# Optimization experiments

Hardware: AMD Instinct MI355X
Metric: run time of the kernel (lower is better)

Reference implementation:

```python
import jax, jax.numpy as jnp
import numpy as np

D_MODEL = 1024
NHEAD = 16
HEAD_DIM = D_MODEL // NHEAD
D_FF = 4096
EPS = 1e-5


def _layer_norm(x, g, b):
    mu = jnp.mean(x, axis=-1, keepdims=True)
    var = jnp.mean((x - mu) ** 2, axis=-1, keepdims=True)
    return (x - mu) * jax.lax.rsqrt(var + EPS) * g + b


def _rotate_every_two(x):
    x1 = x[..., ::2]
    x2 = x[..., 1::2]
    return jnp.stack([-x2, x1], axis=-1).reshape(x.shape)


def _rope_cos_sin(pos_start, length, head_dim, dtype):
    inv_freq = 1.0 / (10000.0 ** (jnp.arange(0, head_dim, 2, dtype=jnp.float32) / head_dim))
    pos = jnp.arange(pos_start, pos_start + length, dtype=jnp.float32)
    ang = jnp.einsum('i,j->ij', pos, inv_freq)  # (len, head_dim/2)
    cos = jnp.repeat(jnp.cos(ang), 2, axis=-1).astype(dtype)
    sin = jnp.repeat(jnp.sin(ang), 2, axis=-1).astype(dtype)
    return cos, sin


def setup_inputs() -> dict:
    key = jax.random.key(0)
    ks = jax.random.split(key, 16)
    s = 1.0 / np.sqrt(D_MODEL)
    sf = 1.0 / np.sqrt(D_FF)
    inp = {
        'src': jax.random.normal(ks[0], (2048, 2, D_MODEL), jnp.float32),
        'src_mask': jnp.ones((2048, 2048), jnp.float32),
        'Wq': jax.random.normal(ks[1], (D_MODEL, D_MODEL), jnp.float32) * s,
        'bq': jnp.zeros((D_MODEL,), jnp.float32),
        'Wk': jax.random.normal(ks[2], (D_MODEL, D_MODEL), jnp.float32) * s,
        'bk': jnp.zeros((D_MODEL,), jnp.float32),
        'Wv': jax.random.normal(ks[3], (D_MODEL, D_MODEL), jnp.float32) * s,
        'bv': jnp.zeros((D_MODEL,), jnp.float32),
        'Wo': jax.random.normal(ks[4], (D_MODEL, D_MODEL), jnp.float32) * s,
        'bo': jnp.zeros((D_MODEL,), jnp.float32),
        'W1': jax.random.normal(ks[5], (D_MODEL, D_FF), jnp.float32) * s,
        'b1': jnp.zeros((D_FF,), jnp.float32),
        'W2': jax.random.normal(ks[6], (D_FF, D_MODEL), jnp.float32) * sf,
        'b2': jnp.zeros((D_MODEL,), jnp.float32),
        'g1': jnp.ones((D_MODEL,), jnp.float32),
        'be1': jnp.zeros((D_MODEL,), jnp.float32),
        'g2': jnp.ones((D_MODEL,), jnp.float32),
        'be2': jnp.zeros((D_MODEL,), jnp.float32),
    }
    return inp


def _attention(q, k, v, attn_mask):
    # q, k, v: (S, B, D) already projected
    s, b, _ = q.shape
    kl = k.shape[0]

    def heads(x):
        # (L, B, D) -> (B, H, L, dh)
        return x.reshape(x.shape[0], b, NHEAD, HEAD_DIM).transpose(1, 2, 0, 3)

    qh, kh, vh = heads(q), heads(k), heads(v)
    q_cos, q_sin = _rope_cos_sin(0, s, HEAD_DIM, qh.dtype)
    k_cos, k_sin = _rope_cos_sin(0, kl, HEAD_DIM, kh.dtype)
    qh = qh * q_cos + _rotate_every_two(qh) * q_sin
    kh = kh * k_cos + _rotate_every_two(kh) * k_sin

    scores = jnp.einsum('bhqd,bhkd->bhqk', qh, kh) / np.sqrt(HEAD_DIM)
    if attn_mask is not None:
        scores = jnp.where(attn_mask[None, None, :, :] < 0.1, -jnp.inf, scores)
    w = jax.nn.softmax(scores, axis=-1)
    out = jnp.einsum('bhqk,bhkd->bhqd', w, vh)  # (B, H, S, dh)
    out = out.transpose(2, 0, 1, 3).reshape(s, b, D_MODEL)
    return out


def reference(src, src_mask, Wq, bq, Wk, bk, Wv, bv, Wo, bo, W1, b1, W2, b2, g1, be1, g2, be2):
    q = src @ Wq + bq
    k = src @ Wk + bk
    v = src @ Wv + bv
    attn = _attention(q, k, v, src_mask) @ Wo + bo
    src2 = _layer_norm(src + attn, g1, be1)
    ff = jax.nn.relu(src2 @ W1 + b1) @ W2 + b2
    out = _layer_norm(src2 + ff, g2, be2)
    return out
```

## Files before the change

kernel.cpp:

```cpp
#include <hip/hip_runtime.h>
#include <math.h>

#define S_LEN 2048
#define DM 1024
#define NH 16
#define HD 64
#define DFF 4096
#define MROWS 4096

typedef unsigned short u16;
typedef __attribute__((ext_vector_type(8))) __bf16 bf16x8;
typedef __attribute__((ext_vector_type(4))) float f32x4;
typedef __attribute__((ext_vector_type(16))) float f32x16;
typedef __attribute__((ext_vector_type(4))) int int32x4;

__device__ __forceinline__ u16 f2bf(float f) {
  unsigned u = __float_as_uint(f);
  unsigned r = (u + 0x7fffu + ((u >> 16) & 1u)) >> 16;
  return (u16)r;
}

__device__ __forceinline__ float bf2f(u16 u) {
  return __uint_as_float((unsigned)u << 16);
}

__device__ __forceinline__ unsigned cvtpk_bf16(float lo, float hi) {
  unsigned r;
  asm("v_cvt_pk_bf16_f32 %0, %1, %2" : "=v"(r) : "v"(lo), "v"(hi));
  return r;
}

__device__ __forceinline__ void gload_lds16(const void* g, void* l) {
  __builtin_amdgcn_global_load_lds((__attribute__((address_space(1))) void*)g,
                                   (__attribute__((address_space(3))) void*)l, 16, 0, 0);
}

__global__ __launch_bounds__(256) void k_prep(const float* __restrict__ Wq, const float* __restrict__ Wk,
                                              const float* __restrict__ Wv, const float* __restrict__ Wo,
                                              const float* __restrict__ W1, const float* __restrict__ W2,
                                              u16* __restrict__ Wq_t, u16* __restrict__ Wk_t,
                                              u16* __restrict__ Wv_t, u16* __restrict__ Wo_t,
                                              u16* __restrict__ W1_t, u16* __restrict__ W2_t,
                                              const float4* __restrict__ src4, ushort4* __restrict__ Xbf4) {
  int flat = blockIdx.x;
  if (flat >= 12288) {
    int i = (flat - 12288) * 256 + threadIdx.x;
    float4 v = src4[i];
    ushort4 o;
    o.x = f2bf(v.x); o.y = f2bf(v.y); o.z = f2bf(v.z); o.w = f2bf(v.w);
    Xbf4[i] = o;
    return;
  }
  __shared__ float tile[32][33];
  const float* W;
  u16* Wt;
  int local, nx, K, N;
  if (flat < 4096) {
    int z = flat >> 10;
    W = z == 0 ? Wq : z == 1 ? Wk : z == 2 ? Wv : Wo;
    Wt = z == 0 ? Wq_t : z == 1 ? Wk_t : z == 2 ? Wv_t : Wo_t;
    local = flat & 1023; nx = 32; K = 1024; N = 1024;
  } else if (flat < 8192) {
    W = W1; Wt = W1_t; local = flat - 4096; nx = 128; K = 1024; N = 4096;
  } else {
    W = W2; Wt = W2_t; local = flat - 8192; nx = 32; K = 4096; N = 1024;
  }
  int n0 = (local % nx) * 32, k0 = (local / nx) * 32;
  int tx = threadIdx.x & 31, ty = threadIdx.x >> 5;
  #pragma unroll
  for (int r = ty; r < 32; r += 8) tile[r][tx] = W[(size_t)(k0 + r) * N + n0 + tx];
  __syncthreads();
  #pragma unroll
  for (int r = ty; r < 32; r += 8) Wt[(size_t)(n0 + r) * K + k0 + tx] = f2bf(tile[tx][r]);
}

__global__ __launch_bounds__(256) void k_misc(float* __restrict__ cosT, float* __restrict__ sinT,
                                              const float* __restrict__ bq, const float* __restrict__ bk,
                                              const float* __restrict__ bv, float* __restrict__ bqkv,
                                              const float* __restrict__ mask,
                                              unsigned char* __restrict__ flags) {
  int flat = blockIdx.x;
  if (flat < 256) {
    int idx = flat * 256 + threadIdx.x;
    int s = idx >> 5, i = idx & 31;
    float inv = powf(10000.f, -(float)(2 * i) / 64.f);
    float ang = (float)s * inv;
    cosT[idx] = cosf(ang);
    sinT[idx] = sinf(ang);
    return;
  }
  if (flat < 268) {
    int i = (flat - 256) * 256 + threadIdx.x;
    if (i < 3072) bqkv[i] = i < 1024 ? bq[i] : (i < 2048 ? bk[i - 1024] : bv[i - 2048]);
    return;
  }
  int local = flat - 268;
  int kt = local & 31, qt = local >> 5;
  const float* mp = mask + (size_t)(qt * 64) * S_LEN + kt * 64;
  int tr = threadIdx.x >> 2;
  int tc = (threadIdx.x & 3) * 16;
  int ok = 1;
  #pragma unroll
  for (int c = 0; c < 16; c += 4) {
    float4 v = *(const float4*)(mp + (size_t)tr * S_LEN + tc + c);
    ok &= (v.x >= 0.1f) & (v.y >= 0.1f) & (v.z >= 0.1f) & (v.w >= 0.1f);
  }
  ok = __all(ok) ? 1 : 0;
  __shared__ int sh[4];
  if ((threadIdx.x & 63) == 0) sh[threadIdx.x >> 6] = ok;
  __syncthreads();
  if (threadIdx.x == 0) flags[qt * 32 + kt] = (sh[0] & sh[1] & sh[2] & sh[3]) ? 0 : 1;
}

enum { EPI_F32 = 0, EPI_RELU_BF16 = 2, EPI_PARTB = 4, EPI_BF16 = 5 };

template <int EPI>
__global__ __launch_bounds__(512, 2) void k_gemm256(const u16* __restrict__ A,
                                                    const u16* __restrict__ Bt,
                                                    const float* __restrict__ bias,
                                                    float* __restrict__ Cf, u16* __restrict__ Cb,
                                                    int M, int N, int K, int ldc, int Kc) {
  __shared__ __attribute__((aligned(16))) u16 As[4][256 * 32];
  __shared__ __attribute__((aligned(16))) u16 Bs[4][256 * 32];

  int nx = gridDim.x;
  int nwg = nx * gridDim.y;
  int flat = blockIdx.y * nx + blockIdx.x;
  int id = (flat & 7) * (nwg >> 3) + (flat >> 3);
  int n0 = (id % nx) * 256;
  int m0 = (id / nx) * 256;
  int kz = blockIdx.z * Kc;

  int tid = threadIdx.x;
  int lane = tid & 63, w = tid >> 6;
  int wm = (w >> 2) * 128, wn = (w & 3) * 64;
  int l15 = lane & 15, l4 = lane >> 4;
  int NT = Kc >> 5;

  const u16* aS[2];
  const u16* bS[2];
  int dslot[2];
  #pragma unroll
  for (int j = 0; j < 2; ++j) {
    int P = j * 512 + tid;
    int r = P >> 2;
    int sl = (P & 3) ^ (r & 3);
    aS[j] = A + (size_t)(m0 + r) * K + kz + sl * 8;
    bS[j] = Bt + (size_t)(n0 + r) * K + kz + sl * 8;
    dslot[j] = j * 512 + w * 64;
  }

  f32x4 acc[8][4] = {};

  #pragma unroll
  for (int t = 0; t < 3; ++t) {
    #pragma unroll
    for (int j = 0; j < 2; ++j) {
      gload_lds16(aS[j] + t * 32, &As[t][dslot[j] * 8]);
      gload_lds16(bS[j] + t * 32, &Bs[t][dslot[j] * 8]);
    }
  }

  for (int t = 0; t < NT; ++t) {
    int buf = t & 3;
    if (t < NT - 2) asm volatile("s_waitcnt vmcnt(8)" ::: "memory");
    else if (t == NT - 2) asm volatile("s_waitcnt vmcnt(4)" ::: "memory");
    else asm volatile("s_waitcnt vmcnt(0)" ::: "memory");
    __builtin_amdgcn_s_barrier();

    if (t + 3 < NT) {
      int tn = t + 3;
      int bn = tn & 3;
      #pragma unroll
      for (int j = 0; j < 2; ++j) {
        gload_lds16(aS[j] + tn * 32, &As[bn][dslot[j] * 8]);
        gload_lds16(bS[j] + tn * 32, &Bs[bn][dslot[j] * 8]);
      }
    }

    bf16x8 af[8], bq[4];
    #pragma unroll
    for (int m = 0; m < 8; ++m) {
      int r = wm + m * 16 + l15;
      af[m] = *(const bf16x8*)&As[buf][r * 32 + (l4 ^ (r & 3)) * 8];
    }
    #pragma unroll
    for (int n = 0; n < 4; ++n) {
      int r = wn + n * 16 + l15;
      bq[n] = *(const bf16x8*)&Bs[buf][r * 32 + (l4 ^ (r & 3)) * 8];
    }
    __builtin_amdgcn_s_setprio(1);
    #pragma unroll
    for (int m = 0; m < 8; ++m)
      #pragma unroll
      for (int n = 0; n < 4; ++n)
        acc[m][n] = __builtin_amdgcn_mfma_f32_16x16x32_bf16(af[m], bq[n], acc[m][n], 0, 0, 0);
    __builtin_amdgcn_s_setprio(0);
  }

  size_t zoff = (size_t)blockIdx.z * M * ldc;
  #pragma unroll
  for (int m = 0; m < 8; ++m) {
    #pragma unroll
    for (int n = 0; n < 4; ++n) {
      int col = n0 + wn + n * 16 + l15;
      float bv = (EPI == EPI_PARTB) ? 0.f : bias[col];
      #pragma unroll
      for (int r = 0; r < 4; ++r) {
        int row = m0 + wm + m * 16 + l4 * 4 + r;
        float v = acc[m][n][r] + bv;
        size_t o = (size_t)row * ldc + col;
        if (EPI == EPI_F32) Cf[o] = v;
        else if (EPI == EPI_RELU_BF16) Cb[o] = f2bf(fmaxf(v, 0.f));
        else if (EPI == EPI_BF16) Cb[o] = f2bf(v);
        else Cb[zoff + o] = f2bf(v);
      }
    }
  }
}

#define QSCALE 0.180336881f
__global__ __launch_bounds__(256) void k_rope_heads(const u16* __restrict__ QKVb,
                                                    const float* __restrict__ cosT,
                                                    const float* __restrict__ sinT,
                                                    u16* __restrict__ Qh, u16* __restrict__ Kh,
                                                    u16* __restrict__ Vt) {
  __shared__ u16 Vlds[64 * 80];
  int bh = blockIdx.y;
  int s0 = blockIdx.x * 64;
  int b = bh >> 4, h = bh & 15;
  int tid = threadIdx.x;
  int sr = tid >> 2, dg = (tid & 3) * 16;
  int s = s0 + sr;
  size_t rowbase = (size_t)(s * 2 + b) * 3072 + h * 64 + dg;

  float4 c0 = *(const float4*)&cosT[s * 32 + (dg >> 1)];
  float4 c1 = *(const float4*)&cosT[s * 32 + (dg >> 1) + 4];
  float4 sn0 = *(const float4*)&sinT[s * 32 + (dg >> 1)];
  float4 sn1 = *(const float4*)&sinT[s * 32 + (dg >> 1) + 4];
  float cs[8] = {c0.x, c0.y, c0.z, c0.w, c1.x, c1.y, c1.z, c1.w};
  float sn[8] = {sn0.x, sn0.y, sn0.z, sn0.w, sn1.x, sn1.y, sn1.z, sn1.w};

  {
    uint4 a = *(const uint4*)&QKVb[rowbase];
    uint4 bbu = *(const uint4*)&QKVb[rowbase + 8];
    unsigned ws[8] = {a.x, a.y, a.z, a.w, bbu.x, bbu.y, bbu.z, bbu.w};
    unsigned o[8];
    #pragma unroll
    for (int j = 0; j < 8; ++j) {
      float lo = bf2f((u16)(ws[j] & 0xffff)), hi = bf2f((u16)(ws[j] >> 16));
      o[j] = cvtpk_bf16((lo * cs[j] - hi * sn[j]) * QSCALE, (hi * cs[j] + lo * sn[j]) * QSCALE);
    }
    u16* qp = &Qh[((size_t)bh * S_LEN + s) * 64 + dg];
    *(uint4*)qp = (uint4){o[0], o[1], o[2], o[3]};
    *(uint4*)(qp + 8) = (uint4){o[4], o[5], o[6], o[7]};
  }
  {
    uint4 a = *(const uint4*)&QKVb[rowbase + 1024];
    uint4 bbu = *(const uint4*)&QKVb[rowbase + 1032];
    unsigned ws[8] = {a.x, a.y, a.z, a.w, bbu.x, bbu.y, bbu.z, bbu.w};
    unsigned o[8];
    #pragma unroll
    for (int j = 0; j < 8; ++j) {
      float lo = bf2f((u16)(ws[j] & 0xffff)), hi = bf2f((u16)(ws[j] >> 16));
      o[j] = cvtpk_bf16(lo * cs[j] - hi * sn[j], hi * cs[j] + lo * sn[j]);
    }
    u16* kp = &Kh[((size_t)bh * S_LEN + s) * 64 + dg];
    *(uint4*)kp = (uint4){o[0], o[1], o[2], o[3]};
    *(uint4*)(kp + 8) = (uint4){o[4], o[5], o[6], o[7]};
  }
  {
    uint4 a = *(const uint4*)&QKVb[rowbase + 2048];
    uint4 bbu = *(const uint4*)&QKVb[rowbase + 2056];
    unsigned ws[8] = {a.x, a.y, a.z, a.w, bbu.x, bbu.y, bbu.z, bbu.w};
    #pragma unroll
    for (int j = 0; j < 8; ++j) {
      Vlds[(dg + 2 * j) * 80 + sr] = (u16)(ws[j] & 0xffff);
      Vlds[(dg + 2 * j + 1) * 80 + sr] = (u16)(ws[j] >> 16);
    }
  }
  __syncthreads();
  {
    int d = tid >> 2, sg = (tid & 3) * 16;
    uint4 v0 = *(const uint4*)&Vlds[d * 80 + sg];
    uint4 v1 = *(const uint4*)&Vlds[d * 80 + sg + 8];
    u16* vp = &Vt[((size_t)bh * 64 + d) * S_LEN + s0 + sg];
    *(uint4*)vp = v0;
    *(uint4*)(vp + 8) = v1;
  }
}

__global__ __launch_bounds__(256) void k_attn(const u16* __restrict__ Qh, const u16* __restrict__ Kh,
                                              const u16* __restrict__ Vt,
                                              const float* __restrict__ mask,
                                              const unsigned char* __restrict__ flags,
                                              u16* __restrict__ Out) {
  __shared__ __attribute__((aligned(16))) u16 Ks[2][128 * 64];
  __shared__ __attribute__((aligned(16))) u16 Vs[2][64 * 128];
  int f = blockIdx.y * gridDim.x + blockIdx.x;
  int xcd = f & 7, ii = f >> 3;
  int bh = xcd * 4 + (ii >> 4);
  int q0 = (ii & 15) * 128;
  int b = bh >> 4, h = bh & 15;
  int tid = threadIdx.x, lane = tid & 63, w = tid >> 6;
  int l31 = lane & 31, l5 = lane >> 5;

  int qrow = q0 + w * 32 + l31;
  int qt = qrow >> 6;

  bf16x8 qf[4];
  {
    const u16* qp = Qh + ((size_t)bh * S_LEN + qrow) * 64 + l5 * 8;
    #pragma unroll
    for (int dc = 0; dc < 4; ++dc) qf[dc] = *(const bf16x8*)(qp + dc * 16);
  }

  const u16* Kbase = Kh + (size_t)bh * S_LEN * 64;
  const u16* Vbase = Vt + (size_t)bh * 64 * S_LEN;

  int ksid[4], vsid[4];
  const u16* kg[4];
  const u16* vg[4];
  #pragma unroll
  for (int i = 0; i < 4; ++i) {
    int sid = i * 256 + tid;
    ksid[i] = sid;
    int kr = sid >> 3, kslot = sid & 7;
    kg[i] = Kbase + (size_t)kr * 64 + (kslot ^ (kr & 7)) * 8;
    vsid[i] = sid;
    int vr = sid >> 4, vslot = sid & 15;
    vg[i] = Vbase + (size_t)vr * S_LEN + ((vslot ^ (vr & 15))) * 8;
  }

  float m_run = -1e30f, l_run = 0.f;
  f32x16 oA = {}, oB = {};

  const int NTILE = S_LEN / 128;
  #pragma unroll
  for (int i = 0; i < 4; ++i) {
    gload_lds16(kg[i], &Ks[0][ksid[i] * 8]);
    gload_lds16(vg[i], &Vs[0][vsid[i] * 8]);
  }

  for (int t = 0; t < NTILE; ++t) {
    int cur = t & 1;
    int kv0 = t * 128;
    asm volatile("s_waitcnt vmcnt(0)" ::: "memory");
    __builtin_amdgcn_s_barrier();
    if (t + 1 < NTILE) {
      int kvn = (t + 1) * 128;
      #pragma unroll
      for (int i = 0; i < 4; ++i) {
        gload_lds16(kg[i] + (size_t)kvn * 64, &Ks[cur ^ 1][ksid[i] * 8]);
        gload_lds16(vg[i] + kvn, &Vs[cur ^ 1][vsid[i] * 8]);
      }
    }

    #pragma unroll
    for (int ksub = 0; ksub < 2; ++ksub) {
      int koff = ksub * 64;
      f32x16 sA = {}, sB = {};
      __builtin_amdgcn_s_setprio(1);
      #pragma unroll
      for (int dc = 0; dc < 4; ++dc) {
        int r0 = koff + l31;
        int r1 = koff + 32 + l31;
        int slot = (dc * 2 + l5) ^ (l31 & 7);
        bf16x8 ka0 = *(const bf16x8*)&Ks[cur][r0 * 64 + slot * 8];
        bf16x8 ka1 = *(const bf16x8*)&Ks[cur][r1 * 64 + slot * 8];
        sA = __builtin_amdgcn_mfma_f32_32x32x16_bf16(ka0, qf[dc], sA, 0, 0, 0);
        sB = __builtin_amdgcn_mfma_f32_32x32x16_bf16(ka1, qf[dc], sB, 0, 0, 0);
      }
      __builtin_amdgcn_s_setprio(0);

      int fl = flags[qt * 32 + ((kv0 + koff) >> 6)];
      if (fl) {
        const float* mrow = mask + (size_t)qrow * S_LEN + kv0 + koff;
        #pragma unroll
        for (int r = 0; r < 16; ++r) {
          int key = (r & 3) + 8 * (r >> 2) + 4 * l5;
          if (mrow[key] < 0.1f) sA[r] = -1e30f;
          if (mrow[key + 32] < 0.1f) sB[r] = -1e30f;
        }
      }

      float pm = m_run;
      #pragma unroll
      for (int r = 0; r < 16; ++r) pm = fmaxf(pm, fmaxf(sA[r], sB[r]));
      pm = fmaxf(pm, __shfl_xor(pm, 32, 64));
      if (!__all(pm <= m_run + 8.f)) {
        float corr = __builtin_amdgcn_exp2f(m_run - pm);
        m_run = pm;
        l_run *= corr;
        #pragma unroll
        for (int r = 0; r < 16; ++r) { oA[r] *= corr; oB[r] *= corr; }
      }
      float ps = 0.f;
      #pragma unroll
      for (int r = 0; r < 16; ++r) {
        sA[r] = __builtin_amdgcn_exp2f(sA[r] - m_run);
        sB[r] = __builtin_amdgcn_exp2f(sB[r] - m_run);
        ps += sA[r] + sB[r];
      }
      l_run += ps;

      __builtin_amdgcn_s_setprio(1);
      #pragma unroll
      for (int kh = 0; kh < 2; ++kh) {
        f32x16 s = kh ? sB : sA;
        #pragma unroll
        for (int c = 0; c < 2; ++c) {
          int base = c * 8;
          unsigned u0 = cvtpk_bf16(s[base + 0], s[base + 1]);
          unsigned u1 = cvtpk_bf16(s[base + 2], s[base + 3]);
          unsigned u2 = cvtpk_bf16(s[base + 4], s[base + 5]);
          unsigned u3 = cvtpk_bf16(s[base + 6], s[base + 7]);
          asm volatile("v_permlane32_swap_b32 %0, %1" : "+v"(u0), "+v"(u2));
          asm volatile("v_permlane32_swap_b32 %0, %1" : "+v"(u1), "+v"(u3));
          int32x4 wds = {(int)u0, (int)u1, (int)u2, (int)u3};
          bf16x8 pb = *(bf16x8*)&wds;
          int kslot = ksub * 8 + (kh * 2 + c) * 2 + l5;
          int vr0 = l31, vr1 = 32 + l31;
          bf16x8 va0 = *(const bf16x8*)&Vs[cur][vr0 * 128 + (kslot ^ (vr0 & 15)) * 8];
          bf16x8 va1 = *(const bf16x8*)&Vs[cur][vr1 * 128 + (kslot ^ (vr1 & 15)) * 8];
          oA = __builtin_amdgcn_mfma_f32_32x32x16_bf16(va0, pb, oA, 0, 0, 0);
          oB = __builtin_amdgcn_mfma_f32_32x32x16_bf16(va1, pb, oB, 0, 0, 0);
        }
      }
      __builtin_amdgcn_s_setprio(0);
    }
  }

  float l_tot = l_run + __shfl_xor(l_run, 32, 64);
  float inv = 1.f / l_tot;
  int mrow = qrow * 2 + b;
  u16* op = Out + (size_t)mrow * DM + h * 64;
  #pragma unroll
  for (int db = 0; db < 2; ++db) {
    f32x16 o = db ? oB : oA;
    #pragma unroll
    for (int g = 0; g < 4; ++g) {
      int d0 = db * 32 + 8 * g + 4 * l5;
      ushort4 st;
      st.x = f2bf(o[4 * g + 0] * inv);
      st.y = f2bf(o[4 * g + 1] * inv);
      st.z = f2bf(o[4 * g + 2] * inv);
      st.w = f2bf(o[4 * g + 3] * inv);
      *(ushort4*)(op + d0) = st;
    }
  }
}

__device__ __forceinline__ float wave_sum(float v) {
  #pragma unroll
  for (int off = 32; off >= 1; off >>= 1) v += __shfl_xor(v, off, 64);
  return v;
}

template <int WB>
__global__ __launch_bounds__(256) void k_lnp(const u16* __restrict__ pb, const float* __restrict__ addf,
                                             const float* __restrict__ bvec,
                                             const float* __restrict__ gw, const float* __restrict__ bw,
                                             float* __restrict__ Yf, u16* __restrict__ Yb) {
  int m = blockIdx.x;
  int tid = threadIdx.x, lane = tid & 63, w = tid >> 6;
  __shared__ float part[4];
  __shared__ float shv[2];
  float4 sc = ((const float4*)(addf + (size_t)m * DM))[tid];
  float4 bv = ((const float4*)bvec)[tid];
  float vx = sc.x + bv.x, vy = sc.y + bv.y, vz = sc.z + bv.z, vw = sc.w + bv.w;
  #pragma unroll
  for (int z = 0; z < 4; ++z) {
    ushort4 qv = ((const ushort4*)(pb + (size_t)z * MROWS * DM + (size_t)m * DM))[tid];
    vx += bf2f(qv.x); vy += bf2f(qv.y); vz += bf2f(qv.z); vw += bf2f(qv.w);
  }
  float s = wave_sum(vx + vy + vz + vw);
  if (lane == 0) part[w] = s;
  __syncthreads();
  if (tid == 0) shv[0] = (part[0] + part[1] + part[2] + part[3]) * (1.f / DM);
  __syncthreads();
  float mu = shv[0];
  float d0 = vx - mu, d1 = vy - mu, d2 = vz - mu, d3 = vw - mu;
  float q = wave_sum(d0 * d0 + d1 * d1 + d2 * d2 + d3 * d3);
  if (lane == 0) part[w] = q;
  __syncthreads();
  if (tid == 0) shv[1] = rsqrtf((part[0] + part[1] + part[2] + part[3]) * (1.f / DM) + 1e-5f);
  __syncthreads();
  float rstd = shv[1];
  float4 g4 = ((const float4*)gw)[tid];
  float4 b4 = ((const float4*)bw)[tid];
  float y0 = d0 * rstd * g4.x + b4.x;
  float y1 = d1 * rstd * g4.y + b4.y;
  float y2 = d2 * rstd * g4.z + b4.z;
  float y3 = d3 * rstd * g4.w + b4.w;
  ((float4*)(Yf + (size_t)m * DM))[tid] = make_float4(y0, y1, y2, y3);
  if (WB) {
    ushort4 o;
    o.x = f2bf(y0); o.y = f2bf(y1); o.z = f2bf(y2); o.w = f2bf(y3);
    ((ushort4*)(Yb + (size_t)m * DM))[tid] = o;
  }
}

extern "C" void kernel_launch(void* const* d_in, const int* in_sizes, int n_in,
                              void* d_out, int out_size, void* d_ws, size_t ws_size,
                              hipStream_t stream) {
  (void)in_sizes; (void)n_in; (void)out_size; (void)ws_size;
  const float* src  = (const float*)d_in[0];
  const float* mask = (const float*)d_in[1];
  const float* Wq = (const float*)d_in[2];  const float* bq  = (const float*)d_in[3];
  const float* Wk = (const float*)d_in[4];  const float* bk  = (const float*)d_in[5];
  const float* Wv = (const float*)d_in[6];  const float* bv  = (const float*)d_in[7];
  const float* Wo = (const float*)d_in[8];  const float* bo  = (const float*)d_in[9];
  const float* W1 = (const float*)d_in[10]; const float* b1  = (const float*)d_in[11];
  const float* W2 = (const float*)d_in[12]; const float* b2  = (const float*)d_in[13];
  const float* g1 = (const float*)d_in[14]; const float* be1 = (const float*)d_in[15];
  const float* g2 = (const float*)d_in[16]; const float* be2 = (const float*)d_in[17];
  float* out = (float*)d_out;

  char* base = (char*)d_ws;
  size_t off = 0;
  auto carve = [&](size_t bytes) -> void* {
    void* r = base + off;
    off += (bytes + 255) & ~(size_t)255;
    return r;
  };
  u16* Wq_t = (u16*)carve(2ull * 1024 * 1024);
  u16* Wk_t = (u16*)carve(2ull * 1024 * 1024);
  u16* Wv_t = (u16*)carve(2ull * 1024 * 1024);
  u16* Wo_t = (u16*)carve(2ull * 1024 * 1024);
  u16* W1_t = (u16*)carve(2ull * 4096 * 1024);
  u16* W2_t = (u16*)carve(2ull * 1024 * 4096);
  u16* Xbf  = (u16*)carve(2ull * 4096 * 1024);
  float* cosT = (float*)carve(4ull * 2048 * 32);
  float* sinT = (float*)carve(4ull * 2048 * 32);
  float* bqkv = (float*)carve(4ull * 3072);
  unsigned char* mflags = (unsigned char*)carve(1024);
  u16* attn_out = (u16*)carve(2ull * 4096 * 1024);
  float* src2f = (float*)carve(4ull * 4096 * 1024);
  float* QKV = (float*)carve(4ull * 4096 * 3072);
  u16* Qh = (u16*)carve(2ull * 32 * 2048 * 64);
  u16* Kh = (u16*)carve(2ull * 32 * 2048 * 64);
  u16* Vt = (u16*)carve(2ull * 32 * 2048 * 64);
  u16* QKVb = (u16*)QKV;
  u16* woPb = (u16*)QKV;
  u16* ff1 = (u16*)QKV;
  u16* ffPb = (u16*)((char*)QKV + 32ull * 1024 * 1024);
  u16* src2b = (u16*)Vt;

  dim3 blk(256);
  dim3 blk5(512);
  k_prep<<<dim3(16384), blk, 0, stream>>>(Wq, Wk, Wv, Wo, W1, W2, Wq_t, Wk_t, Wv_t, Wo_t,
                                          W1_t, W2_t, (const float4*)src, (ushort4*)Xbf);
  k_misc<<<dim3(1292), blk, 0, stream>>>(cosT, sinT, bq, bk, bv, bqkv, mask, mflags);
  k_gemm256<EPI_BF16><<<dim3(12, 16, 1), blk5, 0, stream>>>(Xbf, Wq_t, bqkv, nullptr, QKVb, 4096, 3072, 1024, 3072, 1024);
  k_rope_heads<<<dim3(32, 32), blk, 0, stream>>>(QKVb, cosT, sinT, Qh, Kh, Vt);
  k_attn<<<dim3(16, 32), blk, 0, stream>>>(Qh, Kh, Vt, mask, mflags, attn_out);
  k_gemm256<EPI_PARTB><<<dim3(4, 16, 4), blk5, 0, stream>>>(attn_out, Wo_t, nullptr, nullptr, woPb, 4096, 1024, 1024, 1024, 256);
  k_lnp<1><<<dim3(4096), blk, 0, stream>>>(woPb, src, bo, g1, be1, src2f, src2b);
  k_gemm256<EPI_RELU_BF16><<<dim3(16, 16, 1), blk5, 0, stream>>>(src2b, W1_t, b1, nullptr, ff1, 4096, 4096, 1024, 4096, 1024);
  k_gemm256<EPI_PARTB><<<dim3(4, 16, 4), blk5, 0, stream>>>(ff1, W2_t, nullptr, nullptr, ffPb, 4096, 1024, 4096, 1024, 1024);
  k_lnp<0><<<dim3(4096), blk, 0, stream>>>(ffPb, src2f, b2, g2, be2, out, nullptr);
}
```

Before: 278.1 us.

## Split attention KV tile across two wave groups with LDS merge of partial softmax

The attention kernel now runs 512 threads per block. Two groups of four waves each process one 64-key half of every 128-key tile for the same 128 query rows. The groups keep separate online-softmax state and merge their max, sum and output accumulators through LDS at the end. The global-to-LDS loads are split across the larger block, and the max and sum reductions are tree-shaped. The aim is more waves in flight and shorter dependent chains per tile, at the cost of a final cross-group merge, extra barriers and register pressure under launch_bounds(512,2).

```diff
diff --git a/kernel.cpp b/kernel.cpp
--- a/kernel.cpp
+++ b/kernel.cpp
@@ -290,11 +290,11 @@
   }
 }
 
-__global__ __launch_bounds__(256) void k_attn(const u16* __restrict__ Qh, const u16* __restrict__ Kh,
-                                              const u16* __restrict__ Vt,
-                                              const float* __restrict__ mask,
-                                              const unsigned char* __restrict__ flags,
-                                              u16* __restrict__ Out) {
+__global__ __launch_bounds__(512, 2) void k_attn(const u16* __restrict__ Qh, const u16* __restrict__ Kh,
+                                                 const u16* __restrict__ Vt,
+                                                 const float* __restrict__ mask,
+                                                 const unsigned char* __restrict__ flags,
+                                                 u16* __restrict__ Out) {
   __shared__ __attribute__((aligned(16))) u16 Ks[2][128 * 64];
   __shared__ __attribute__((aligned(16))) u16 Vs[2][64 * 128];
   int f = blockIdx.y * gridDim.x + blockIdx.x;
@@ -303,9 +303,10 @@
   int q0 = (ii & 15) * 128;
   int b = bh >> 4, h = bh & 15;
   int tid = threadIdx.x, lane = tid & 63, w = tid >> 6;
+  int wq = w & 3, wh = w >> 2;
   int l31 = lane & 31, l5 = lane >> 5;
 
-  int qrow = q0 + w * 32 + l31;
+  int qrow = q0 + wq * 32 + l31;
   int qt = qrow >> 6;
 
   bf16x8 qf[4];
@@ -318,18 +319,14 @@
   const u16* Kbase = Kh + (size_t)bh * S_LEN * 64;
   const u16* Vbase = Vt + (size_t)bh * 64 * S_LEN;
 
-  int ksid[4], vsid[4];
-  const u16* kg[4];
-  const u16* vg[4];
-  #pragma unroll
-  for (int i = 0; i < 4; ++i) {
-    int sid = i * 256 + tid;
-    ksid[i] = sid;
-    int kr = sid >> 3, kslot = sid & 7;
-    kg[i] = Kbase + (size_t)kr * 64 + (kslot ^ (kr & 7)) * 8;
-    vsid[i] = sid;
-    int vr = sid >> 4, vslot = sid & 15;
-    vg[i] = Vbase + (size_t)vr * S_LEN + ((vslot ^ (vr & 15))) * 8;
+  int koff_[2], voff_[2];
+  #pragma unroll
+  for (int i = 0; i < 2; ++i) {
+    int s = i * 512 + tid;
+    int kr = s >> 3, kslot = s & 7;
+    koff_[i] = kr * 64 + (kslot ^ (kr & 7)) * 8;
+    int vr = s >> 4, vslot = s & 15;
+    voff_[i] = vr * S_LEN + (vslot ^ (vr & 15)) * 8;
   }
 
   float m_run = -1e30f, l_run = 0.f;
@@ -337,116 +334,144 @@
 
   const int NTILE = S_LEN / 128;
   #pragma unroll
-  for (int i = 0; i < 4; ++i) {
-    gload_lds16(kg[i], &Ks[0][ksid[i] * 8]);
-    gload_lds16(vg[i], &Vs[0][vsid[i] * 8]);
-  }
+  for (int i = 0; i < 2; ++i) {
+    gload_lds16(Kbase + koff_[i], &Ks[0][(i * 512 + tid) * 8]);
+    gload_lds16(Vbase + voff_[i], &Vs[0][(i * 512 + tid) * 8]);
+  }
+
+  int khalf = wh * 64;
 
   for (int t = 0; t < NTILE; ++t) {
     int cur = t & 1;
-    int kv0 = t * 128;
     asm volatile("s_waitcnt vmcnt(0)" ::: "memory");
     __builtin_amdgcn_s_barrier();
     if (t + 1 < NTILE) {
-      int kvn = (t + 1) * 128;
-      #pragma unroll
-      for (int i = 0; i < 4; ++i) {
-        gload_lds16(kg[i] + (size_t)kvn * 64, &Ks[cur ^ 1][ksid[i] * 8]);
-        gload_lds16(vg[i] + kvn, &Vs[cur ^ 1][vsid[i] * 8]);
+      const u16* kt_ = Kbase + (size_t)(t + 1) * 8192;
+      const u16* vt_ = Vbase + (t + 1) * 128;
+      #pragma unroll
+      for (int i = 0; i < 2; ++i) {
+        gload_lds16(kt_ + koff_[i], &Ks[cur ^ 1][(i * 512 + tid) * 8]);
+        gload_lds16(vt_ + voff_[i], &Vs[cur ^ 1][(i * 512 + tid) * 8]);
       }
     }
 
-    #pragma unroll
-    for (int ksub = 0; ksub < 2; ++ksub) {
-      int koff = ksub * 64;
-      f32x16 sA = {}, sB = {};
-      __builtin_amdgcn_s_setprio(1);
-      #pragma unroll
-      for (int dc = 0; dc < 4; ++dc) {
-        int r0 = koff + l31;
-        int r1 = koff + 32 + l31;
-        int slot = (dc * 2 + l5) ^ (l31 & 7);
-        bf16x8 ka0 = *(const bf16x8*)&Ks[cur][r0 * 64 + slot * 8];
-        bf16x8 ka1 = *(const bf16x8*)&Ks[cur][r1 * 64 + slot * 8];
-        sA = __builtin_amdgcn_mfma_f32_32x32x16_bf16(ka0, qf[dc], sA, 0, 0, 0);
-        sB = __builtin_amdgcn_mfma_f32_32x32x16_bf16(ka1, qf[dc], sB, 0, 0, 0);
+    f32x16 sA = {}, sB = {};
+    __builtin_amdgcn_s_setprio(1);
+    #pragma unroll
+    for (int dc = 0; dc < 4; ++dc) {
+      int r0 = khalf + l31, r1 = khalf + 32 + l31;
+      int slot = (dc * 2 + l5) ^ (l31 & 7);
+      bf16x8 ka0 = *(const bf16x8*)&Ks[cur][r0 * 64 + slot * 8];
+      bf16x8 ka1 = *(const bf16x8*)&Ks[cur][r1 * 64 + slot * 8];
+      sA = __builtin_amdgcn_mfma_f32_32x32x16_bf16(ka0, qf[dc], sA, 0, 0, 0);
+      sB = __builtin_amdgcn_mfma_f32_32x32x16_bf16(ka1, qf[dc], sB, 0, 0, 0);
+    }
+    __builtin_amdgcn_s_setprio(0);
+
+    int kv0abs = t * 128 + khalf;
+    int fl = flags[qt * 32 + (kv0abs >> 6)];
+    if (fl) {
+      const float* mrow = mask + (size_t)qrow * S_LEN + kv0abs;
+      #pragma unroll
+      for (int r = 0; r < 16; ++r) {
+        int key = (r & 3) + 8 * (r >> 2) + 4 * l5;
+        if (mrow[key] < 0.1f) sA[r] = -1e30f;
+        if (mrow[key + 32] < 0.1f) sB[r] = -1e30f;
       }
-      __builtin_amdgcn_s_setprio(0);
-
-      int fl = flags[qt * 32 + ((kv0 + koff) >> 6)];
-      if (fl) {
-        const float* mrow = mask + (size_t)qrow * S_LEN + kv0 + koff;
-        #pragma unroll
-        for (int r = 0; r < 16; ++r) {
-          int key = (r & 3) + 8 * (r >> 2) + 4 * l5;
-          if (mrow[key] < 0.1f) sA[r] = -1e30f;
-          if (mrow[key + 32] < 0.1f) sB[r] = -1e30f;
-        }
+    }
+
+    float mx8[8];
+    #pragma unroll
+    for (int r = 0; r < 8; ++r)
+      mx8[r] = fmaxf(fmaxf(sA[r], sA[r + 8]), fmaxf(sB[r], sB[r + 8]));
+    #pragma unroll
+    for (int r = 0; r < 4; ++r) mx8[r] = fmaxf(mx8[r], mx8[r + 4]);
+    float pm = fmaxf(fmaxf(fmaxf(mx8[0], mx8[1]), fmaxf(mx8[2], mx8[3])), m_run);
+    pm = fmaxf(pm, __shfl_xor(pm, 32, 64));
+    if (!__all(pm <= m_run + 8.f)) {
+      float corr = __builtin_amdgcn_exp2f(m_run - pm);
+      m_run = pm;
+      l_run *= corr;
+      #pragma unroll
+      for (int r = 0; r < 16; ++r) { oA[r] *= corr; oB[r] *= corr; }
+    }
+    #pragma unroll
+    for (int r = 0; r < 16; ++r) {
+      sA[r] = __builtin_amdgcn_exp2f(sA[r] - m_run);
+      sB[r] = __builtin_amdgcn_exp2f(sB[r] - m_run);
+    }
+    float t8[8];
+    #pragma unroll
+    for (int r = 0; r < 8; ++r) t8[r] = (sA[r] + sA[r + 8]) + (sB[r] + sB[r + 8]);
+    #pragma unroll
+    for (int r = 0; r < 4; ++r) t8[r] += t8[r + 4];
+    l_run += (t8[0] + t8[1]) + (t8[2] + t8[3]);
+
+    __builtin_amdgcn_s_setprio(1);
+    #pragma unroll
+    for (int kh = 0; kh < 2; ++kh) {
+      f32x16 s = kh ? sB : sA;
+      #pragma unroll
+      for (int c = 0; c < 2; ++c) {
+        int base = c * 8;
+        unsigned u0 = cvtpk_bf16(s[base + 0], s[base + 1]);
+        unsigned u1 = cvtpk_bf16(s[base + 2], s[base + 3]);
+        unsigned u2 = cvtpk_bf16(s[base + 4], s[base + 5]);
+        unsigned u3 = cvtpk_bf16(s[base + 6], s[base + 7]);
+        asm volatile("v_permlane32_swap_b32 %0, %1" : "+v"(u0), "+v"(u2));
+        asm volatile("v_permlane32_swap_b32 %0, %1" : "+v"(u1), "+v"(u3));
+        int32x4 wds = {(int)u0, (int)u1, (int)u2, (int)u3};
+        bf16x8 pb = *(bf16x8*)&wds;
+        int kslot = wh * 8 + (kh * 2 + c) * 2 + l5;
+        int vr0 = l31, vr1 = 32 + l31;
+        bf16x8 va0 = *(const bf16x8*)&Vs[cur][vr0 * 128 + (kslot ^ (vr0 & 15)) * 8];
+        bf16x8 va1 = *(const bf16x8*)&Vs[cur][vr1 * 128 + (kslot ^ (vr1 & 15)) * 8];
+        oA = __builtin_amdgcn_mfma_f32_32x32x16_bf16(va0, pb, oA, 0, 0, 0);
+        oB = __builtin_amdgcn_mfma_f32_32x32x16_bf16(va1, pb, oB, 0, 0, 0);
       }
-
-      float pm = m_run;
-      #pragma unroll
-      for (int r = 0; r < 16; ++r) pm = fmaxf(pm, fmaxf(sA[r], sB[r]));
-      pm = fmaxf(pm, __shfl_xor(pm, 32, 64));
-      if (!__all(pm <= m_run + 8.f)) {
-        float corr = __builtin_amdgcn_exp2f(m_run - pm);
-        m_run = pm;
-        l_run *= corr;
-        #pragma unroll
-        for (int r = 0; r < 16; ++r) { oA[r] *= corr; oB[r] *= corr; }
+    }
+    __builtin_amdgcn_s_setprio(0);
+  }
+
+  float l_tot = l_run + __shfl_xor(l_run, 32, 64);
+  __syncthreads();
+  float* mlds = (float*)Vs;
+  mlds[w * 64 + lane] = m_run;
+  mlds[512 + w * 64 + lane] = l_tot;
+  __syncthreads();
+  int pw = w ^ 4;
+  float pm2 = mlds[pw * 64 + lane];
+  float pl2 = mlds[512 + pw * 64 + lane];
+  float M = fmaxf(m_run, pm2);
+  float wgt = __builtin_amdgcn_exp2f(m_run - M);
+  float pwgt = __builtin_amdgcn_exp2f(pm2 - M);
+  float denom = l_tot * wgt + pl2 * pwgt;
+  float* oxc = (float*)Ks;
+  if (wh == 1) {
+    #pragma unroll
+    for (int r = 0; r < 16; ++r) {
+      oxc[r * 256 + wq * 64 + lane] = oA[r] * wgt;
+      oxc[(16 + r) * 256 + wq * 64 + lane] = oB[r] * wgt;
+    }
+  }
+  __syncthreads();
+  if (wh == 0) {
+    float inv = 1.f / denom;
+    int mrow = qrow * 2 + b;
+    u16* op = Out + (size_t)mrow * DM + h * 64;
+    #pragma unroll
+    for (int db = 0; db < 2; ++db) {
+      f32x16 o = db ? oB : oA;
+      #pragma unroll
+      for (int g = 0; g < 4; ++g) {
+        int d0 = db * 32 + 8 * g + 4 * l5;
+        ushort4 st;
+        st.x = f2bf((o[4 * g + 0] * wgt + oxc[(db * 16 + 4 * g + 0) * 256 + wq * 64 + lane]) * inv);
+        st.y = f2bf((o[4 * g + 1] * wgt + oxc[(db * 16 + 4 * g + 1) * 256 + wq * 64 + lane]) * inv);
+        st.z = f2bf((o[4 * g + 2] * wgt + oxc[(db * 16 + 4 * g + 2) * 256 + wq * 64 + lane]) * inv);
+        st.w = f2bf((o[4 * g + 3] * wgt + oxc[(db * 16 + 4 * g + 3) * 256 + wq * 64 + lane]) * inv);
+        *(ushort4*)(op + d0) = st;
       }
-      float ps = 0.f;
-      #pragma unroll
-      for (int r = 0; r < 16; ++r) {
-        sA[r] = __builtin_amdgcn_exp2f(sA[r] - m_run);
-        sB[r] = __builtin_amdgcn_exp2f(sB[r] - m_run);
-        ps += sA[r] + sB[r];
-      }
-      l_run += ps;
-
-      __builtin_amdgcn_s_setprio(1);
-      #pragma unroll
-      for (int kh = 0; kh < 2; ++kh) {
-        f32x16 s = kh ? sB : sA;
-        #pragma unroll
-        for (int c = 0; c < 2; ++c) {
-          int base = c * 8;
-          unsigned u0 = cvtpk_bf16(s[base + 0], s[base + 1]);
-          unsigned u1 = cvtpk_bf16(s[base + 2], s[base + 3]);
-          unsigned u2 = cvtpk_bf16(s[base + 4], s[base + 5]);
-          unsigned u3 = cvtpk_bf16(s[base + 6], s[base + 7]);
-          asm volatile("v_permlane32_swap_b32 %0, %1" : "+v"(u0), "+v"(u2));
-          asm volatile("v_permlane32_swap_b32 %0, %1" : "+v"(u1), "+v"(u3));
-          int32x4 wds = {(int)u0, (int)u1, (int)u2, (int)u3};
-          bf16x8 pb = *(bf16x8*)&wds;
-          int kslot = ksub * 8 + (kh * 2 + c) * 2 + l5;
-          int vr0 = l31, vr1 = 32 + l31;
-          bf16x8 va0 = *(const bf16x8*)&Vs[cur][vr0 * 128 + (kslot ^ (vr0 & 15)) * 8];
-          bf16x8 va1 = *(const bf16x8*)&Vs[cur][vr1 * 128 + (kslot ^ (vr1 & 15)) * 8];
-          oA = __builtin_amdgcn_mfma_f32_32x32x16_bf16(va0, pb, oA, 0, 0, 0);
-          oB = __builtin_amdgcn_mfma_f32_32x32x16_bf16(va1, pb, oB, 0, 0, 0);
-        }
-      }
-      __builtin_amdgcn_s_setprio(0);
-    }
-  }
-
-  float l_tot = l_run + __shfl_xor(l_run, 32, 64);
-  float inv = 1.f / l_tot;
-  int mrow = qrow * 2 + b;
-  u16* op = Out + (size_t)mrow * DM + h * 64;
-  #pragma unroll
-  for (int db = 0; db < 2; ++db) {
-    f32x16 o = db ? oB : oA;
-    #pragma unroll
-    for (int g = 0; g < 4; ++g) {
-      int d0 = db * 32 + 8 * g + 4 * l5;
-      ushort4 st;
-      st.x = f2bf(o[4 * g + 0] * inv);
-      st.y = f2bf(o[4 * g + 1] * inv);
-      st.z = f2bf(o[4 * g + 2] * inv);
-      st.w = f2bf(o[4 * g + 3] * inv);
-      *(ushort4*)(op + d0) = st;
     }
   }
 }
@@ -554,7 +579,7 @@
   k_misc<<<dim3(1292), blk, 0, stream>>>(cosT, sinT, bq, bk, bv, bqkv, mask, mflags);
   k_gemm256<EPI_BF16><<<dim3(12, 16, 1), blk5, 0, stream>>>(Xbf, Wq_t, bqkv, nullptr, QKVb, 4096, 3072, 1024, 3072, 1024);
   k_rope_heads<<<dim3(32, 32), blk, 0, stream>>>(QKVb, cosT, sinT, Qh, Kh, Vt);
-  k_attn<<<dim3(16, 32), blk, 0, stream>>>(Qh, Kh, Vt, mask, mflags, attn_out);
+  k_attn<<<dim3(16, 32), blk5, 0, stream>>>(Qh, Kh, Vt, mask, mflags, attn_out);
   k_gemm256<EPI_PARTB><<<dim3(4, 16, 4), blk5, 0, stream>>>(attn_out, Wo_t, nullptr, nullptr, woPb, 4096, 1024, 1024, 1024, 256);
   k_lnp<1><<<dim3(4096), blk, 0, stream>>>(woPb, src, bo, g1, be1, src2f, src2b);
   k_gemm256<EPI_RELU_BF16><<<dim3(16, 16, 1), blk5, 0, stream>>>(src2b, W1_t, b1, nullptr, ff1, 4096, 4096, 1024, 4096, 1024);
```

Result: slower. 286.1 us (+2.9%).

## Merge misc prep into k_prep and deepen attention K/V pipeline to 4 stages

Applied to the files above, without the earlier changes.

Folds the rope table, bias concatenation and mask-flag work of k_misc into the k_prep launch, saving one kernel launch. The attention kernel moves from double-buffered 128-key tiles to a 4-slot ring of 64-key tiles with three tiles in flight, using graded vmcnt waits. Each tile now takes a single barrier, and the max and sum reductions become tree-shaped. Smaller tiles mean more barriers per row, but loads get more latency hiding; LDS use stays the same.

```diff
diff --git a/kernel.cpp b/kernel.cpp
--- a/kernel.cpp
+++ b/kernel.cpp
@@ -41,8 +41,46 @@
                                               u16* __restrict__ Wq_t, u16* __restrict__ Wk_t,
                                               u16* __restrict__ Wv_t, u16* __restrict__ Wo_t,
                                               u16* __restrict__ W1_t, u16* __restrict__ W2_t,
-                                              const float4* __restrict__ src4, ushort4* __restrict__ Xbf4) {
+                                              const float4* __restrict__ src4, ushort4* __restrict__ Xbf4,
+                                              float* __restrict__ cosT, float* __restrict__ sinT,
+                                              const float* __restrict__ bq, const float* __restrict__ bk,
+                                              const float* __restrict__ bv, float* __restrict__ bqkv,
+                                              const float* __restrict__ mask,
+                                              unsigned char* __restrict__ flags) {
   int flat = blockIdx.x;
+  if (flat >= 16652) {
+    int local = flat - 16652;
+    int kt = local & 31, qt = local >> 5;
+    const float* mp = mask + (size_t)(qt * 64) * S_LEN + kt * 64;
+    int tr = threadIdx.x >> 2;
+    int tc = (threadIdx.x & 3) * 16;
+    int ok = 1;
+    #pragma unroll
+    for (int c = 0; c < 16; c += 4) {
+      float4 v = *(const float4*)(mp + (size_t)tr * S_LEN + tc + c);
+      ok &= (v.x >= 0.1f) & (v.y >= 0.1f) & (v.z >= 0.1f) & (v.w >= 0.1f);
+    }
+    ok = __all(ok) ? 1 : 0;
+    __shared__ int sh[4];
+    if ((threadIdx.x & 63) == 0) sh[threadIdx.x >> 6] = ok;
+    __syncthreads();
+    if (threadIdx.x == 0) flags[qt * 32 + kt] = (sh[0] & sh[1] & sh[2] & sh[3]) ? 0 : 1;
+    return;
+  }
+  if (flat >= 16640) {
+    int i = (flat - 16640) * 256 + threadIdx.x;
+    if (i < 3072) bqkv[i] = i < 1024 ? bq[i] : (i < 2048 ? bk[i - 1024] : bv[i - 2048]);
+    return;
+  }
+  if (flat >= 16384) {
+    int idx = (flat - 16384) * 256 + threadIdx.x;
+    int s = idx >> 5, i = idx & 31;
+    float inv = powf(10000.f, -(float)(2 * i) / 64.f);
+    float ang = (float)s * inv;
+    cosT[idx] = cosf(ang);
+    sinT[idx] = sinf(ang);
+    return;
+  }
   if (flat >= 12288) {
     int i = (flat - 12288) * 256 + threadIdx.x;
     float4 v = src4[i];
@@ -72,44 +110,6 @@
   __syncthreads();
   #pragma unroll
   for (int r = ty; r < 32; r += 8) Wt[(size_t)(n0 + r) * K + k0 + tx] = f2bf(tile[tx][r]);
-}
-
-__global__ __launch_bounds__(256) void k_misc(float* __restrict__ cosT, float* __restrict__ sinT,
-                                              const float* __restrict__ bq, const float* __restrict__ bk,
-                                              const float* __restrict__ bv, float* __restrict__ bqkv,
-                                              const float* __restrict__ mask,
-                                              unsigned char* __restrict__ flags) {
-  int flat = blockIdx.x;
-  if (flat < 256) {
-    int idx = flat * 256 + threadIdx.x;
-    int s = idx >> 5, i = idx & 31;
-    float inv = powf(10000.f, -(float)(2 * i) / 64.f);
-    float ang = (float)s * inv;
-    cosT[idx] = cosf(ang);
-    sinT[idx] = sinf(ang);
-    return;
-  }
-  if (flat < 268) {
-    int i = (flat - 256) * 256 + threadIdx.x;
-    if (i < 3072) bqkv[i] = i < 1024 ? bq[i] : (i < 2048 ? bk[i - 1024] : bv[i - 2048]);
-    return;
-  }
-  int local = flat - 268;
-  int kt = local & 31, qt = local >> 5;
-  const float* mp = mask + (size_t)(qt * 64) * S_LEN + kt * 64;
-  int tr = threadIdx.x >> 2;
-  int tc = (threadIdx.x & 3) * 16;
-  int ok = 1;
-  #pragma unroll
-  for (int c = 0; c < 16; c += 4) {
-    float4 v = *(const float4*)(mp + (size_t)tr * S_LEN + tc + c);
-    ok &= (v.x >= 0.1f) & (v.y >= 0.1f) & (v.z >= 0.1f) & (v.w >= 0.1f);
-  }
-  ok = __all(ok) ? 1 : 0;
-  __shared__ int sh[4];
-  if ((threadIdx.x & 63) == 0) sh[threadIdx.x >> 6] = ok;
-  __syncthreads();
-  if (threadIdx.x == 0) flags[qt * 32 + kt] = (sh[0] & sh[1] & sh[2] & sh[3]) ? 0 : 1;
 }
 
 enum { EPI_F32 = 0, EPI_RELU_BF16 = 2, EPI_PARTB = 4, EPI_BF16 = 5 };
@@ -295,8 +295,8 @@
                                               const float* __restrict__ mask,
                                               const unsigned char* __restrict__ flags,
                                               u16* __restrict__ Out) {
-  __shared__ __attribute__((aligned(16))) u16 Ks[2][128 * 64];
-  __shared__ __attribute__((aligned(16))) u16 Vs[2][64 * 128];
+  __shared__ __attribute__((aligned(16))) u16 Ks[4][64 * 64];
+  __shared__ __attribute__((aligned(16))) u16 Vs[4][64 * 64];
   int f = blockIdx.y * gridDim.x + blockIdx.x;
   int xcd = f & 7, ii = f >> 3;
   int bh = xcd * 4 + (ii >> 4);
@@ -318,117 +318,121 @@
   const u16* Kbase = Kh + (size_t)bh * S_LEN * 64;
   const u16* Vbase = Vt + (size_t)bh * 64 * S_LEN;
 
-  int ksid[4], vsid[4];
-  const u16* kg[4];
-  const u16* vg[4];
-  #pragma unroll
-  for (int i = 0; i < 4; ++i) {
-    int sid = i * 256 + tid;
-    ksid[i] = sid;
-    int kr = sid >> 3, kslot = sid & 7;
-    kg[i] = Kbase + (size_t)kr * 64 + (kslot ^ (kr & 7)) * 8;
-    vsid[i] = sid;
-    int vr = sid >> 4, vslot = sid & 15;
-    vg[i] = Vbase + (size_t)vr * S_LEN + ((vslot ^ (vr & 15))) * 8;
+  int koff_[2], voff_[2], dsl_[2];
+  #pragma unroll
+  for (int i = 0; i < 2; ++i) {
+    int s = i * 256 + tid;
+    dsl_[i] = s;
+    int kr = s >> 3, ksl = s & 7;
+    koff_[i] = kr * 64 + (ksl ^ (kr & 7)) * 8;
+    int vr = s >> 3, vsl = s & 7;
+    voff_[i] = vr * S_LEN + (vsl ^ (vr & 7)) * 8;
   }
 
   float m_run = -1e30f, l_run = 0.f;
   f32x16 oA = {}, oB = {};
 
-  const int NTILE = S_LEN / 128;
-  #pragma unroll
-  for (int i = 0; i < 4; ++i) {
-    gload_lds16(kg[i], &Ks[0][ksid[i] * 8]);
-    gload_lds16(vg[i], &Vs[0][vsid[i] * 8]);
-  }
-
-  for (int t = 0; t < NTILE; ++t) {
-    int cur = t & 1;
-    int kv0 = t * 128;
-    asm volatile("s_waitcnt vmcnt(0)" ::: "memory");
+  const int NT = S_LEN / 64;
+  #pragma unroll
+  for (int t = 0; t < 3; ++t) {
+    #pragma unroll
+    for (int i = 0; i < 2; ++i) {
+      gload_lds16(Kbase + t * 4096 + koff_[i], &Ks[t][dsl_[i] * 8]);
+      gload_lds16(Vbase + t * 64 + voff_[i], &Vs[t][dsl_[i] * 8]);
+    }
+  }
+
+  for (int t = 0; t < NT; ++t) {
+    int cur = t & 3;
+    if (t < NT - 2) asm volatile("s_waitcnt vmcnt(8)" ::: "memory");
+    else if (t == NT - 2) asm volatile("s_waitcnt vmcnt(4)" ::: "memory");
+    else asm volatile("s_waitcnt vmcnt(0)" ::: "memory");
     __builtin_amdgcn_s_barrier();
-    if (t + 1 < NTILE) {
-      int kvn = (t + 1) * 128;
-      #pragma unroll
-      for (int i = 0; i < 4; ++i) {
-        gload_lds16(kg[i] + (size_t)kvn * 64, &Ks[cur ^ 1][ksid[i] * 8]);
-        gload_lds16(vg[i] + kvn, &Vs[cur ^ 1][vsid[i] * 8]);
+
+    if (t + 3 < NT) {
+      int bn = (t + 3) & 3;
+      #pragma unroll
+      for (int i = 0; i < 2; ++i) {
+        gload_lds16(Kbase + (size_t)(t + 3) * 4096 + koff_[i], &Ks[bn][dsl_[i] * 8]);
+        gload_lds16(Vbase + (t + 3) * 64 + voff_[i], &Vs[bn][dsl_[i] * 8]);
       }
     }
 
-    #pragma unroll
-    for (int ksub = 0; ksub < 2; ++ksub) {
-      int koff = ksub * 64;
-      f32x16 sA = {}, sB = {};
-      __builtin_amdgcn_s_setprio(1);
-      #pragma unroll
-      for (int dc = 0; dc < 4; ++dc) {
-        int r0 = koff + l31;
-        int r1 = koff + 32 + l31;
-        int slot = (dc * 2 + l5) ^ (l31 & 7);
-        bf16x8 ka0 = *(const bf16x8*)&Ks[cur][r0 * 64 + slot * 8];
-        bf16x8 ka1 = *(const bf16x8*)&Ks[cur][r1 * 64 + slot * 8];
-        sA = __builtin_amdgcn_mfma_f32_32x32x16_bf16(ka0, qf[dc], sA, 0, 0, 0);
-        sB = __builtin_amdgcn_mfma_f32_32x32x16_bf16(ka1, qf[dc], sB, 0, 0, 0);
+    f32x16 sA = {}, sB = {};
+    __builtin_amdgcn_s_setprio(1);
+    #pragma unroll
+    for (int dc = 0; dc < 4; ++dc) {
+      int r0 = l31, r1 = 32 + l31;
+      int slot = dc * 2 + l5;
+      bf16x8 ka0 = *(const bf16x8*)&Ks[cur][r0 * 64 + (slot ^ (r0 & 7)) * 8];
+      bf16x8 ka1 = *(const bf16x8*)&Ks[cur][r1 * 64 + (slot ^ (r1 & 7)) * 8];
+      sA = __builtin_amdgcn_mfma_f32_32x32x16_bf16(ka0, qf[dc], sA, 0, 0, 0);
+      sB = __builtin_amdgcn_mfma_f32_32x32x16_bf16(ka1, qf[dc], sB, 0, 0, 0);
+    }
+    __builtin_amdgcn_s_setprio(0);
+
+    int fl = flags[qt * 32 + t];
+    if (fl) {
+      const float* mrow = mask + (size_t)qrow * S_LEN + t * 64;
+      #pragma unroll
+      for (int r = 0; r < 16; ++r) {
+        int key = (r & 3) + 8 * (r >> 2) + 4 * l5;
+        if (mrow[key] < 0.1f) sA[r] = -1e30f;
+        if (mrow[key + 32] < 0.1f) sB[r] = -1e30f;
       }
-      __builtin_amdgcn_s_setprio(0);
-
-      int fl = flags[qt * 32 + ((kv0 + koff) >> 6)];
-      if (fl) {
-        const float* mrow = mask + (size_t)qrow * S_LEN + kv0 + koff;
-        #pragma unroll
-        for (int r = 0; r < 16; ++r) {
-          int key = (r & 3) + 8 * (r >> 2) + 4 * l5;
-          if (mrow[key] < 0.1f) sA[r] = -1e30f;
-          if (mrow[key + 32] < 0.1f) sB[r] = -1e30f;
-        }
+    }
+
+    float mx8[8];
+    #pragma unroll
+    for (int r = 0; r < 8; ++r)
+      mx8[r] = fmaxf(fmaxf(sA[r], sA[r + 8]), fmaxf(sB[r], sB[r + 8]));
+    #pragma unroll
+    for (int r = 0; r < 4; ++r) mx8[r] = fmaxf(mx8[r], mx8[r + 4]);
+    float pm = fmaxf(fmaxf(fmaxf(mx8[0], mx8[1]), fmaxf(mx8[2], mx8[3])), m_run);
+    pm = fmaxf(pm, __shfl_xor(pm, 32, 64));
+    if (!__all(pm <= m_run + 8.f)) {
+      float corr = __builtin_amdgcn_exp2f(m_run - pm);
+      m_run = pm;
+      l_run *= corr;
+      #pragma unroll
+      for (int r = 0; r < 16; ++r) { oA[r] *= corr; oB[r] *= corr; }
+    }
+    #pragma unroll
+    for (int r = 0; r < 16; ++r) {
+      sA[r] = __builtin_amdgcn_exp2f(sA[r] - m_run);
+      sB[r] = __builtin_amdgcn_exp2f(sB[r] - m_run);
+    }
+    float t8[8];
+    #pragma unroll
+    for (int r = 0; r < 8; ++r) t8[r] = (sA[r] + sA[r + 8]) + (sB[r] + sB[r + 8]);
+    #pragma unroll
+    for (int r = 0; r < 4; ++r) t8[r] += t8[r + 4];
+    l_run += (t8[0] + t8[1]) + (t8[2] + t8[3]);
+
+    __builtin_amdgcn_s_setprio(1);
+    #pragma unroll
+    for (int kh = 0; kh < 2; ++kh) {
+      f32x16 s = kh ? sB : sA;
+      #pragma unroll
+      for (int c = 0; c < 2; ++c) {
+        int base = c * 8;
+        unsigned u0 = cvtpk_bf16(s[base + 0], s[base + 1]);
+        unsigned u1 = cvtpk_bf16(s[base + 2], s[base + 3]);
+        unsigned u2 = cvtpk_bf16(s[base + 4], s[base + 5]);
+        unsigned u3 = cvtpk_bf16(s[base + 6], s[base + 7]);
+        asm volatile("v_permlane32_swap_b32 %0, %1" : "+v"(u0), "+v"(u2));
+        asm volatile("v_permlane32_swap_b32 %0, %1" : "+v"(u1), "+v"(u3));
+        int32x4 wds = {(int)u0, (int)u1, (int)u2, (int)u3};
+        bf16x8 pb = *(bf16x8*)&wds;
+        int kslot = (kh * 2 + c) * 2 + l5;
+        int vr0 = l31, vr1 = 32 + l31;
+        bf16x8 va0 = *(const bf16x8*)&Vs[cur][vr0 * 64 + (kslot ^ (vr0 & 7)) * 8];
+        bf16x8 va1 = *(const bf16x8*)&Vs[cur][vr1 * 64 + (kslot ^ (vr1 & 7)) * 8];
+        oA = __builtin_amdgcn_mfma_f32_32x32x16_bf16(va0, pb, oA, 0, 0, 0);
+        oB = __builtin_amdgcn_mfma_f32_32x32x16_bf16(va1, pb, oB, 0, 0, 0);
       }
-
-      float pm = m_run;
-      #pragma unroll
-      for (int r = 0; r < 16; ++r) pm = fmaxf(pm, fmaxf(sA[r], sB[r]));
-      pm = fmaxf(pm, __shfl_xor(pm, 32, 64));
-      if (!__all(pm <= m_run + 8.f)) {
-        float corr = __builtin_amdgcn_exp2f(m_run - pm);
-        m_run = pm;
-        l_run *= corr;
-        #pragma unroll
-        for (int r = 0; r < 16; ++r) { oA[r] *= corr; oB[r] *= corr; }
-      }
-      float ps = 0.f;
-      #pragma unroll
-      for (int r = 0; r < 16; ++r) {
-        sA[r] = __builtin_amdgcn_exp2f(sA[r] - m_run);
-        sB[r] = __builtin_amdgcn_exp2f(sB[r] - m_run);
-        ps += sA[r] + sB[r];
-      }
-      l_run += ps;
-
-      __builtin_amdgcn_s_setprio(1);
-      #pragma unroll
-      for (int kh = 0; kh < 2; ++kh) {
-        f32x16 s = kh ? sB : sA;
-        #pragma unroll
-        for (int c = 0; c < 2; ++c) {
-          int base = c * 8;
-          unsigned u0 = cvtpk_bf16(s[base + 0], s[base + 1]);
-          unsigned u1 = cvtpk_bf16(s[base + 2], s[base + 3]);
-          unsigned u2 = cvtpk_bf16(s[base + 4], s[base + 5]);
-          unsigned u3 = cvtpk_bf16(s[base + 6], s[base + 7]);
-          asm volatile("v_permlane32_swap_b32 %0, %1" : "+v"(u0), "+v"(u2));
-          asm volatile("v_permlane32_swap_b32 %0, %1" : "+v"(u1), "+v"(u3));
-          int32x4 wds = {(int)u0, (int)u1, (int)u2, (int)u3};
-          bf16x8 pb = *(bf16x8*)&wds;
-          int kslot = ksub * 8 + (kh * 2 + c) * 2 + l5;
-          int vr0 = l31, vr1 = 32 + l31;
-          bf16x8 va0 = *(const bf16x8*)&Vs[cur][vr0 * 128 + (kslot ^ (vr0 & 15)) * 8];
-          bf16x8 va1 = *(const bf16x8*)&Vs[cur][vr1 * 128 + (kslot ^ (vr1 & 15)) * 8];
-          oA = __builtin_amdgcn_mfma_f32_32x32x16_bf16(va0, pb, oA, 0, 0, 0);
-          oB = __builtin_amdgcn_mfma_f32_32x32x16_bf16(va1, pb, oB, 0, 0, 0);
-        }
-      }
-      __builtin_amdgcn_s_setprio(0);
-    }
+    }
+    __builtin_amdgcn_s_setprio(0);
   }
 
   float l_tot = l_run + __shfl_xor(l_run, 32, 64);
@@ -549,9 +553,9 @@
 
   dim3 blk(256);
   dim3 blk5(512);
-  k_prep<<<dim3(16384), blk, 0, stream>>>(Wq, Wk, Wv, Wo, W1, W2, Wq_t, Wk_t, Wv_t, Wo_t,
-                                          W1_t, W2_t, (const float4*)src, (ushort4*)Xbf);
-  k_misc<<<dim3(1292), blk, 0, stream>>>(cosT, sinT, bq, bk, bv, bqkv, mask, mflags);
+  k_prep<<<dim3(17676), blk, 0, stream>>>(Wq, Wk, Wv, Wo, W1, W2, Wq_t, Wk_t, Wv_t, Wo_t,
+                                          W1_t, W2_t, (const float4*)src, (ushort4*)Xbf,
+                                          cosT, sinT, bq, bk, bv, bqkv, mask, mflags);
   k_gemm256<EPI_BF16><<<dim3(12, 16, 1), blk5, 0, stream>>>(Xbf, Wq_t, bqkv, nullptr, QKVb, 4096, 3072, 1024, 3072, 1024);
   k_rope_heads<<<dim3(32, 32), blk, 0, stream>>>(QKVb, cosT, sinT, Qh, Kh, Vt);
   k_attn<<<dim3(16, 32), blk, 0, stream>>>(Qh, Kh, Vt, mask, mflags, attn_out);
```

After: 283.9 us. 2.1% more time.
